# Performance work log

Hardware: AMD Instinct MI355X
Metric: run time of the kernel (lower is better)

## Reference

```python
import jax, jax.numpy as jnp
import numpy as np

N_NODES = 100000
N_EDGES = 800000
IN_CH = 128
HID = 128
OUT_CH = 64


def setup_inputs() -> dict:
    key = jax.random.key(0)
    ks = jax.random.split(key, 8)
    x = jax.random.normal(ks[0], (N_NODES, IN_CH), dtype=jnp.float32)
    edge_index = jax.random.randint(ks[1], (2, N_EDGES), 0, N_NODES, dtype=jnp.int64)
    # GCNConv weights (Glorot) and zero biases
    def glorot(k, fan_in, fan_out):
        s = jnp.sqrt(6.0 / (fan_in + fan_out))
        return jax.random.uniform(k, (fan_in, fan_out), jnp.float32, -s, s)
    return {
        "x": x,
        "edge_index": edge_index,
        "W1": glorot(ks[2], IN_CH, HID), "b1": jnp.zeros((HID,), jnp.float32),
        "W2": glorot(ks[3], HID, HID),   "b2": jnp.zeros((HID,), jnp.float32),
        "W3": glorot(ks[4], HID, OUT_CH), "b3": jnp.zeros((OUT_CH,), jnp.float32),
    }


def _gcn_conv(h, W, b, src, dst, norm, self_norm, n_nodes):
    """PyG GCNConv: out = D^-1/2 (A+I) D^-1/2 (h W) + b.
    Self-loop contribution added densely (self_norm = dinv^2) to avoid
    appending N extra edges."""
    h = h @ W  # [N, F_out]
    msg = h[src] * norm[:, None]  # [E, F_out] gathered + normalized messages
    agg = jax.ops.segment_sum(msg, dst, num_segments=n_nodes)
    return agg + h * self_norm[:, None] + b


def reference(x, edge_index, W1, b1, W2, b2, W3, b3):
    n_nodes = x.shape[0]
    src = edge_index[0]
    dst = edge_index[1]
    # degrees with self-loops (edge weights = 1)
    deg = jax.ops.segment_sum(jnp.ones_like(src, dtype=x.dtype), dst,
                              num_segments=n_nodes) + 1.0
    dinv = jax.lax.rsqrt(deg)
    norm = dinv[src] * dinv[dst]   # per-edge symmetric normalization
    self_norm = dinv * dinv        # normalization of the i->i self loop

    h = jax.nn.relu(_gcn_conv(x, W1, b1, src, dst, norm, self_norm, n_nodes))
    # dropout is identity in eval mode (training=False)
    h = jax.nn.relu(_gcn_conv(h, W2, b2, src, dst, norm, self_norm, n_nodes))
    out = _gcn_conv(h, W3, b3, src, dst, norm, self_norm, n_nodes)
    return out
```

## Files before the change

### kernel.cpp

```cpp
#include <hip/hip_runtime.h>


#define IN_CH 128

typedef __attribute__((ext_vector_type(8))) short bf16x8;
typedef __attribute__((ext_vector_type(4))) float f32x4;

__device__ inline unsigned short f2bf_rne(float f) {
    unsigned u = __float_as_uint(f);
    unsigned r = (u + 0x7FFFu + ((u >> 16) & 1u)) >> 16;
    return (unsigned short)r;
}
__device__ inline float bf2f(unsigned short h) {
    return __uint_as_float(((unsigned)h) << 16);
}
__device__ inline float bf2f_lo(unsigned m) {
    return __uint_as_float(m << 16);
}
__device__ inline float bf2f_hi(unsigned m) {
    return __uint_as_float(m & 0xffff0000u);
}

__global__ __launch_bounds__(256) void cnt_k(const int* __restrict__ dst,
                                             int* __restrict__ cnt, int E) {
    int e = blockIdx.x * 256 + threadIdx.x;
    if (e < E) atomicAdd(&cnt[dst[e]], 1);
}

__global__ __launch_bounds__(256) void scan1_k(const int* __restrict__ cnt,
                                               int* __restrict__ bsum,
                                               float* __restrict__ dinv, int N) {
    __shared__ int s[256];
    int tid = threadIdx.x;
    int i = blockIdx.x * 256 + tid;
    int vr = (i < N) ? cnt[i] : 0;
    if (i < N) dinv[i] = rsqrtf((float)vr + 1.0f);
    s[tid] = (i < N) ? ((vr + 8) & ~7) : 0;
    __syncthreads();
    for (int off = 128; off > 0; off >>= 1) {
        if (tid < off) s[tid] += s[tid + off];
        __syncthreads();
    }
    if (tid == 0) bsum[blockIdx.x] = s[0];
}

__global__ __launch_bounds__(512) void scan2_k(int* __restrict__ bsum, int nb) {
    __shared__ int s[512];
    __shared__ int carry_s;
    int tid = threadIdx.x;
    if (tid == 0) carry_s = 0;
    __syncthreads();
    for (int base = 0; base < nb; base += 512) {
        int c = carry_s;
        int i = base + tid;
        int v = (i < nb) ? bsum[i] : 0;
        s[tid] = v;
        __syncthreads();
        for (int off = 1; off < 512; off <<= 1) {
            int t = (tid >= off) ? s[tid - off] : 0;
            __syncthreads();
            s[tid] += t;
            __syncthreads();
        }
        if (i < nb) bsum[i] = s[tid] - v + c;
        __syncthreads();
        if (tid == 0) carry_s = c + s[511];
        __syncthreads();
    }
}

__global__ __launch_bounds__(256) void scan3_k(const int* __restrict__ cnt,
                                               const int* __restrict__ bsum,
                                               int* __restrict__ rowstart,
                                               int* __restrict__ cur, int N) {
    __shared__ int s[256];
    int tid = threadIdx.x;
    int i = blockIdx.x * 256 + tid;
    int v = (i < N) ? ((cnt[i] + 8) & ~7) : 0;
    s[tid] = v;
    __syncthreads();
    for (int off = 1; off < 256; off <<= 1) {
        int t = (tid >= off) ? s[tid - off] : 0;
        __syncthreads();
        s[tid] += t;
        __syncthreads();
    }
    if (i < N) {
        int st = s[tid] - v + bsum[blockIdx.x];
        rowstart[i] = st;
        cur[i] = st;
        if (i == N - 1) rowstart[N] = st + v;
    }
}

__device__ inline void convw_one(const float* W, unsigned short* hi, int FOUT, int id) {
    int n = id >> 7, k = id & 127;
    hi[id] = f2bf_rne(W[k * FOUT + n]);
}

__global__ __launch_bounds__(256) void fill_conv_k(
    const int* __restrict__ src, const int* __restrict__ dst,
    const float* __restrict__ dinv, int* __restrict__ cur,
    int2* __restrict__ pairs, int E, int N, int fillBlocks, int selfBlocks,
    int rangeSz,
    const float* __restrict__ W1, const float* __restrict__ W2,
    const float* __restrict__ W3,
    unsigned short* __restrict__ W1h, unsigned short* __restrict__ W2h,
    unsigned short* __restrict__ W3h) {
    if ((int)blockIdx.x < fillBlocks) {
        const int range = blockIdx.x & 7;
        const int lo = range * rangeSz;
        const int hi = lo + rangeSz;
        const int e0 = (blockIdx.x >> 3) * 1024 + threadIdx.x * 4;
        if (e0 >= E) return;
        int s[4], d[4];
        if (e0 + 4 <= E) {
            int4 s4 = *(const int4*)(src + e0);
            int4 d4 = *(const int4*)(dst + e0);
            s[0] = s4.x; s[1] = s4.y; s[2] = s4.z; s[3] = s4.w;
            d[0] = d4.x; d[1] = d4.y; d[2] = d4.z; d[3] = d4.w;
        } else {
#pragma unroll
            for (int k = 0; k < 4; ++k) {
                s[k] = (e0 + k < E) ? src[e0 + k] : 0;
                d[k] = (e0 + k < E) ? dst[e0 + k] : -1;
            }
        }
#pragma unroll
        for (int k = 0; k < 4; ++k) {
            if (d[k] >= lo && d[k] < hi) {
                float nrm = dinv[s[k]] * dinv[d[k]];
                int pos = atomicAdd(&cur[d[k]], 1);
                pairs[pos] = make_int2(s[k] * 256, __float_as_int(nrm));
            }
        }
    } else if ((int)blockIdx.x < fillBlocks + selfBlocks) {
        int i = (blockIdx.x - fillBlocks) * 256 + threadIdx.x;
        if (i < N) {
            float di = dinv[i];
            int pos = atomicAdd(&cur[i], 1);
            pairs[pos] = make_int2(i * 256, __float_as_int(di * di));
        }
    } else {
        int id = (blockIdx.x - fillBlocks - selfBlocks) * 256 + threadIdx.x;
        if (id < 16384) convw_one(W1, W1h, 128, id);
        else if (id < 32768) convw_one(W2, W2h, 128, id - 16384);
        else if (id < 40960) convw_one(W3, W3h, 64, id - 32768);
    }
}

__device__ inline bf16x8 cvt8(const float* __restrict__ p) {
    float4 v0 = *(const float4*)p;
    float4 v1 = *(const float4*)(p + 4);
    bf16x8 h;
    h[0] = (short)f2bf_rne(v0.x); h[1] = (short)f2bf_rne(v0.y);
    h[2] = (short)f2bf_rne(v0.z); h[3] = (short)f2bf_rne(v0.w);
    h[4] = (short)f2bf_rne(v1.x); h[5] = (short)f2bf_rne(v1.y);
    h[6] = (short)f2bf_rne(v1.z); h[7] = (short)f2bf_rne(v1.w);
    return h;
}

template <int FOUT, bool AF32>
__global__ __launch_bounds__(256) void mfma_gemm(const float* __restrict__ Af,
                                                 const unsigned short* __restrict__ Ahi,
                                                 const unsigned short* __restrict__ Bhi,
                                                 unsigned short* __restrict__ Thi,
                                                 int N) {
    constexpr int NCT = FOUT / 16;
    constexpr int BSTRIDE = 136;
    constexpr int CSTRIDE = FOUT + 8;
    constexpr int BU = FOUT * BSTRIDE;
    constexpr int CU = 64 * CSTRIDE;
    constexpr int SMEMU = (BU > CU) ? BU : CU;
    __shared__ unsigned short smem[SMEMU];

    const int tid = threadIdx.x;
    const int wv = tid >> 6, lane = tid & 63;
    const int quad = lane >> 4, l16 = lane & 15;
    const int row0 = blockIdx.x * 64 + wv * 16;

#pragma unroll
    for (int it = 0; it < FOUT / 16; ++it) {
        int i = it * 256 + tid;
        int r = i >> 4, c = (i & 15) * 8;
        *(bf16x8*)(&smem[r * BSTRIDE + c]) = *(const bf16x8*)(Bhi + (size_t)r * 128 + c);
    }
    __syncthreads();

    f32x4 acc[NCT];
#pragma unroll
    for (int ct = 0; ct < NCT; ++ct)
        acc[ct] = (f32x4){0.f, 0.f, 0.f, 0.f};

    const int ra = AF32 ? min(row0 + l16, N - 1) : (row0 + l16);

#pragma unroll
    for (int ks = 0; ks < 4; ++ks) {
        const int ko = ks * 32 + quad * 8;
        bf16x8 ah;
        if (AF32) {
            ah = cvt8(Af + (size_t)ra * 128 + ko);
        } else {
            ah = *(const bf16x8*)(Ahi + (size_t)ra * 128 + ko);
        }
#pragma unroll
        for (int ct = 0; ct < NCT; ++ct) {
            bf16x8 bh = *(const bf16x8*)(&smem[(ct * 16 + l16) * BSTRIDE + ko]);
            acc[ct] = __builtin_amdgcn_mfma_f32_16x16x32_bf16(ah, bh, acc[ct], 0, 0, 0);
        }
    }

    __syncthreads();
    const int lrow = wv * 16 + quad * 4;
#pragma unroll
    for (int ct = 0; ct < NCT; ++ct) {
        const int col = ct * 16 + l16;
#pragma unroll
        for (int r = 0; r < 4; ++r)
            smem[(lrow + r) * CSTRIDE + col] = f2bf_rne(acc[ct][r]);
    }
    __syncthreads();
    constexpr int CH = FOUT / 8;
#pragma unroll
    for (int i = 0; i < 64 * CH / 256; ++i) {
        int ci = i * 256 + tid;
        int r = ci / CH, c = (ci % CH) * 8;
        int grow = blockIdx.x * 64 + r;
        if (grow < N)
            *(uint4*)(Thi + (size_t)grow * FOUT + c) = *(const uint4*)&smem[r * CSTRIDE + c];
    }
}

struct Pairs4 { int4 p0, p1, p2, p3; };

__device__ inline Pairs4 ldpairs(const int2* __restrict__ pairs, int j) {
    Pairs4 r;
    r.p0 = *(const int4*)(pairs + j);
    r.p1 = *(const int4*)(pairs + j + 2);
    r.p2 = *(const int4*)(pairs + j + 4);
    r.p3 = *(const int4*)(pairs + j + 6);
    return r;
}

__device__ inline void ldrows128(const char* __restrict__ tbase, int laneB,
                                 const Pairs4& P, unsigned m[8]) {
    m[0] = *(const unsigned*)(tbase + (unsigned)P.p0.x + laneB);
    m[1] = *(const unsigned*)(tbase + (unsigned)P.p0.z + laneB);
    m[2] = *(const unsigned*)(tbase + (unsigned)P.p1.x + laneB);
    m[3] = *(const unsigned*)(tbase + (unsigned)P.p1.z + laneB);
    m[4] = *(const unsigned*)(tbase + (unsigned)P.p2.x + laneB);
    m[5] = *(const unsigned*)(tbase + (unsigned)P.p2.z + laneB);
    m[6] = *(const unsigned*)(tbase + (unsigned)P.p3.x + laneB);
    m[7] = *(const unsigned*)(tbase + (unsigned)P.p3.z + laneB);
}

__device__ inline void fma8_128(const Pairs4& P, const unsigned m[8],
                                float& ax, float& ay) {
    float n0 = __int_as_float(P.p0.y), n1 = __int_as_float(P.p0.w);
    float n2 = __int_as_float(P.p1.y), n3 = __int_as_float(P.p1.w);
    float n4 = __int_as_float(P.p2.y), n5 = __int_as_float(P.p2.w);
    float n6 = __int_as_float(P.p3.y), n7 = __int_as_float(P.p3.w);
    ax += n0 * bf2f_lo(m[0]); ay += n0 * bf2f_hi(m[0]);
    ax += n1 * bf2f_lo(m[1]); ay += n1 * bf2f_hi(m[1]);
    ax += n2 * bf2f_lo(m[2]); ay += n2 * bf2f_hi(m[2]);
    ax += n3 * bf2f_lo(m[3]); ay += n3 * bf2f_hi(m[3]);
    ax += n4 * bf2f_lo(m[4]); ay += n4 * bf2f_hi(m[4]);
    ax += n5 * bf2f_lo(m[5]); ay += n5 * bf2f_hi(m[5]);
    ax += n6 * bf2f_lo(m[6]); ay += n6 * bf2f_hi(m[6]);
    ax += n7 * bf2f_lo(m[7]); ay += n7 * bf2f_hi(m[7]);
}

__device__ inline void ldrows64(const char* __restrict__ tbase, int laneB,
                                const Pairs4& P, float m[8]) {
    m[0] = bf2f(*(const unsigned short*)(tbase + ((unsigned)P.p0.x >> 1) + laneB));
    m[1] = bf2f(*(const unsigned short*)(tbase + ((unsigned)P.p0.z >> 1) + laneB));
    m[2] = bf2f(*(const unsigned short*)(tbase + ((unsigned)P.p1.x >> 1) + laneB));
    m[3] = bf2f(*(const unsigned short*)(tbase + ((unsigned)P.p1.z >> 1) + laneB));
    m[4] = bf2f(*(const unsigned short*)(tbase + ((unsigned)P.p2.x >> 1) + laneB));
    m[5] = bf2f(*(const unsigned short*)(tbase + ((unsigned)P.p2.z >> 1) + laneB));
    m[6] = bf2f(*(const unsigned short*)(tbase + ((unsigned)P.p3.x >> 1) + laneB));
    m[7] = bf2f(*(const unsigned short*)(tbase + ((unsigned)P.p3.z >> 1) + laneB));
}

__device__ inline void fma8_64(const Pairs4& P, const float m[8], float& acc) {
    acc += __int_as_float(P.p0.y) * m[0] + __int_as_float(P.p0.w) * m[1] +
           __int_as_float(P.p1.y) * m[2] + __int_as_float(P.p1.w) * m[3] +
           __int_as_float(P.p2.y) * m[4] + __int_as_float(P.p2.w) * m[5] +
           __int_as_float(P.p3.y) * m[6] + __int_as_float(P.p3.w) * m[7];
}

template <int FOUT, bool SPLIT>
__global__ __launch_bounds__(256) void gather_k(const int* __restrict__ rowstart,
                                                const int2* __restrict__ pairs,
                                                const unsigned short* __restrict__ Thi,
                                                const float* __restrict__ bias,
                                                float* __restrict__ out,
                                                unsigned short* __restrict__ outHi,
                                                int N) {
    const int wave = threadIdx.x >> 6;
    const int lane = threadIdx.x & 63;
    const int rowA = blockIdx.x * 8 + wave * 2;
    if (rowA >= N) return;
    const int rowB = rowA + 1;
    const bool hasB = rowB < N;

    int2 se = *(const int2*)(rowstart + rowA);
    const int startA = se.x, endA = se.y;
    const int startB = endA;
    const int endB = hasB ? rowstart[rowA + 2] : startB;
    const char* tbase = (const char*)Thi;

    int itA = (endA - startA) >> 3;
    int itB = (endB - startB) >> 3;
    const int c = min(itA, itB);

    if (FOUT == 128) {
        const int laneB = lane * 4;
        float2 bb = *(const float2*)(bias + lane * 2);
        float axA = bb.x, ayA = bb.y, axB = bb.x, ayB = bb.y;

        Pairs4 PA = ldpairs(pairs, startA);
        Pairs4 PB = {};
        if (hasB) PB = ldpairs(pairs, startB);
        int jA = startA, jB = startB;

        for (int t = 0; t < c; ++t) {
            unsigned mA[8], mB[8];
            ldrows128(tbase, laneB, PA, mA);
            ldrows128(tbase, laneB, PB, mB);
            jA += 8; jB += 8;
            Pairs4 QA = ldpairs(pairs, jA);
            Pairs4 QB = ldpairs(pairs, jB);
            fma8_128(PA, mA, axA, ayA);
            fma8_128(PB, mB, axB, ayB);
            PA = QA; PB = QB;
        }
        for (int t = c; t < itA; ++t) {
            unsigned mA[8];
            ldrows128(tbase, laneB, PA, mA);
            jA += 8;
            Pairs4 QA = ldpairs(pairs, jA);
            fma8_128(PA, mA, axA, ayA);
            PA = QA;
        }
        for (int t = c; t < itB; ++t) {
            unsigned mB[8];
            ldrows128(tbase, laneB, PB, mB);
            jB += 8;
            Pairs4 QB = ldpairs(pairs, jB);
            fma8_128(PB, mB, axB, ayB);
            PB = QB;
        }

        if (SPLIT) {
            ushort2 hA;
            hA.x = f2bf_rne(fmaxf(axA, 0.f));
            hA.y = f2bf_rne(fmaxf(ayA, 0.f));
            *(ushort2*)(outHi + (size_t)rowA * 128 + lane * 2) = hA;
            if (hasB) {
                ushort2 hB;
                hB.x = f2bf_rne(fmaxf(axB, 0.f));
                hB.y = f2bf_rne(fmaxf(ayB, 0.f));
                *(ushort2*)(outHi + (size_t)rowB * 128 + lane * 2) = hB;
            }
        } else {
            float2 oA; oA.x = axA; oA.y = ayA;
            *(float2*)(out + (size_t)rowA * 128 + lane * 2) = oA;
            if (hasB) {
                float2 oB; oB.x = axB; oB.y = ayB;
                *(float2*)(out + (size_t)rowB * 128 + lane * 2) = oB;
            }
        }
    } else {
        const int laneB = lane * 2;
        const float bb = bias[lane];
        float accA = bb, accB = bb;

        Pairs4 PA = ldpairs(pairs, startA);
        Pairs4 PB = {};
        if (hasB) PB = ldpairs(pairs, startB);
        int jA = startA, jB = startB;

        for (int t = 0; t < c; ++t) {
            float mA[8], mB[8];
            ldrows64(tbase, laneB, PA, mA);
            ldrows64(tbase, laneB, PB, mB);
            jA += 8; jB += 8;
            Pairs4 QA = ldpairs(pairs, jA);
            Pairs4 QB = ldpairs(pairs, jB);
            fma8_64(PA, mA, accA);
            fma8_64(PB, mB, accB);
            PA = QA; PB = QB;
        }
        for (int t = c; t < itA; ++t) {
            float mA[8];
            ldrows64(tbase, laneB, PA, mA);
            jA += 8;
            Pairs4 QA = ldpairs(pairs, jA);
            fma8_64(PA, mA, accA);
            PA = QA;
        }
        for (int t = c; t < itB; ++t) {
            float mB[8];
            ldrows64(tbase, laneB, PB, mB);
            jB += 8;
            Pairs4 QB = ldpairs(pairs, jB);
            fma8_64(PB, mB, accB);
            PB = QB;
        }

        out[(size_t)rowA * FOUT + lane] = accA;
        if (hasB) out[(size_t)rowB * FOUT + lane] = accB;
    }
}

extern "C" void kernel_launch(void* const* d_in, const int* in_sizes, int n_in,
                              void* d_out, int out_size, void* d_ws, size_t ws_size,
                              hipStream_t stream) {
    const float* x  = (const float*)d_in[0];
    const int* eidx = (const int*)d_in[1];
    const float* W1 = (const float*)d_in[2];
    const float* b1 = (const float*)d_in[3];
    const float* W2 = (const float*)d_in[4];
    const float* b2 = (const float*)d_in[5];
    const float* W3 = (const float*)d_in[6];
    const float* b3 = (const float*)d_in[7];
    float* out = (float*)d_out;

    const int N = in_sizes[0] / IN_CH;
    const int E = in_sizes[1] / 2;
    const int* src = eidx;
    const int* dst = eidx + E;
    const int Npad = ((N + 127) / 128) * 128;
    const int nb = (N + 255) / 256;
    const int Emax = E + 8 * N + 24;

    auto align = [](size_t v) { return (v + 255) / 256 * 256; };
    char* p = (char*)d_ws;
    int* cnt = (int*)p;            p += align((size_t)N * 4);
    int* rowstart = (int*)p;       p += align((size_t)(N + 1) * 4);
    int* cur = (int*)p;            p += align((size_t)N * 4);
    int* bsum = (int*)p;           p += align((size_t)nb * 4);
    float* dinv = (float*)p;       p += align((size_t)N * 4);
    int2* pairs = (int2*)p;        p += align((size_t)Emax * 8);
    unsigned short* Ahi = (unsigned short*)p;  p += align((size_t)Npad * 128 * 2);
    unsigned short* Thi = (unsigned short*)p;  p += align((size_t)Npad * 128 * 2);
    unsigned short* W1h = (unsigned short*)p;  p += align(128 * 128 * 2);
    unsigned short* W2h = (unsigned short*)p;  p += align(128 * 128 * 2);
    unsigned short* W3h = (unsigned short*)p;

    hipMemsetAsync(cnt, 0, (size_t)N * 4, stream);
    hipMemsetAsync(pairs, 0, (size_t)Emax * 8, stream);
    cnt_k<<<(E + 255) / 256, 256, 0, stream>>>(dst, cnt, E);
    scan1_k<<<nb, 256, 0, stream>>>(cnt, bsum, dinv, N);
    scan2_k<<<1, 512, 0, stream>>>(bsum, nb);
    scan3_k<<<nb, 256, 0, stream>>>(cnt, bsum, rowstart, cur, N);
    const int chunks = (E + 1023) / 1024;
    const int fillBlocks = chunks * 8;
    const int selfBlocks = (N + 255) / 256;
    const int rangeSz = (N + 7) / 8;
    fill_conv_k<<<fillBlocks + selfBlocks + 160, 256, 0, stream>>>(
        src, dst, dinv, cur, pairs, E, N, fillBlocks, selfBlocks, rangeSz,
        W1, W2, W3, W1h, W2h, W3h);

    const int gemm_blocks = (N + 63) / 64;
    const int gather_blocks = (N + 7) / 8;

    mfma_gemm<128, true><<<gemm_blocks, 256, 0, stream>>>(x, nullptr, W1h, Thi, N);
    gather_k<128, true><<<gather_blocks, 256, 0, stream>>>(rowstart, pairs, Thi,
                                                           b1, nullptr, Ahi, N);
    mfma_gemm<128, false><<<gemm_blocks, 256, 0, stream>>>(nullptr, Ahi, W2h, Thi, N);
    gather_k<128, true><<<gather_blocks, 256, 0, stream>>>(rowstart, pairs, Thi,
                                                           b2, nullptr, Ahi, N);
    mfma_gemm<64, false><<<gemm_blocks, 256, 0, stream>>>(nullptr, Ahi, W3h, Thi, N);
    gather_k<64, false><<<gather_blocks, 256, 0, stream>>>(rowstart, pairs, Thi,
                                                           b3, out, nullptr, N);
}
```

Baseline: 350.6 us.

## Fuse first GEMM with CSR fill and make gather grid-stride

```diff
diff --git a/kernel.cpp b/kernel.cpp
--- a/kernel.cpp
+++ b/kernel.cpp
@@ -21,10 +21,26 @@
     return __uint_as_float(m & 0xffff0000u);
 }
 
-__global__ __launch_bounds__(256) void cnt_k(const int* __restrict__ dst,
-                                             int* __restrict__ cnt, int E) {
-    int e = blockIdx.x * 256 + threadIdx.x;
-    if (e < E) atomicAdd(&cnt[dst[e]], 1);
+__device__ inline void convw_one(const float* W, unsigned short* hi, int FOUT, int id) {
+    int n = id >> 7, k = id & 127;
+    hi[id] = f2bf_rne(W[k * FOUT + n]);
+}
+
+__global__ __launch_bounds__(256) void cntconv_k(
+    const int* __restrict__ dst, int* __restrict__ cnt, int E, int cntBlocks,
+    const float* __restrict__ W1, const float* __restrict__ W2,
+    const float* __restrict__ W3,
+    unsigned short* __restrict__ W1h, unsigned short* __restrict__ W2h,
+    unsigned short* __restrict__ W3h) {
+    if ((int)blockIdx.x < cntBlocks) {
+        int e = blockIdx.x * 256 + threadIdx.x;
+        if (e < E) atomicAdd(&cnt[dst[e]], 1);
+    } else {
+        int id = (blockIdx.x - cntBlocks) * 256 + threadIdx.x;
+        if (id < 16384) convw_one(W1, W1h, 128, id);
+        else if (id < 32768) convw_one(W2, W2h, 128, id - 16384);
+        else if (id < 40960) convw_one(W3, W3h, 64, id - 32768);
+    }
 }
 
 __global__ __launch_bounds__(256) void scan1_k(const int* __restrict__ cnt,
@@ -93,62 +109,6 @@
     }
 }
 
-__device__ inline void convw_one(const float* W, unsigned short* hi, int FOUT, int id) {
-    int n = id >> 7, k = id & 127;
-    hi[id] = f2bf_rne(W[k * FOUT + n]);
-}
-
-__global__ __launch_bounds__(256) void fill_conv_k(
-    const int* __restrict__ src, const int* __restrict__ dst,
-    const float* __restrict__ dinv, int* __restrict__ cur,
-    int2* __restrict__ pairs, int E, int N, int fillBlocks, int selfBlocks,
-    int rangeSz,
-    const float* __restrict__ W1, const float* __restrict__ W2,
-    const float* __restrict__ W3,
-    unsigned short* __restrict__ W1h, unsigned short* __restrict__ W2h,
-    unsigned short* __restrict__ W3h) {
-    if ((int)blockIdx.x < fillBlocks) {
-        const int range = blockIdx.x & 7;
-        const int lo = range * rangeSz;
-        const int hi = lo + rangeSz;
-        const int e0 = (blockIdx.x >> 3) * 1024 + threadIdx.x * 4;
-        if (e0 >= E) return;
-        int s[4], d[4];
-        if (e0 + 4 <= E) {
-            int4 s4 = *(const int4*)(src + e0);
-            int4 d4 = *(const int4*)(dst + e0);
-            s[0] = s4.x; s[1] = s4.y; s[2] = s4.z; s[3] = s4.w;
-            d[0] = d4.x; d[1] = d4.y; d[2] = d4.z; d[3] = d4.w;
-        } else {
-#pragma unroll
-            for (int k = 0; k < 4; ++k) {
-                s[k] = (e0 + k < E) ? src[e0 + k] : 0;
-                d[k] = (e0 + k < E) ? dst[e0 + k] : -1;
-            }
-        }
-#pragma unroll
-        for (int k = 0; k < 4; ++k) {
-            if (d[k] >= lo && d[k] < hi) {
-                float nrm = dinv[s[k]] * dinv[d[k]];
-                int pos = atomicAdd(&cur[d[k]], 1);
-                pairs[pos] = make_int2(s[k] * 256, __float_as_int(nrm));
-            }
-        }
-    } else if ((int)blockIdx.x < fillBlocks + selfBlocks) {
-        int i = (blockIdx.x - fillBlocks) * 256 + threadIdx.x;
-        if (i < N) {
-            float di = dinv[i];
-            int pos = atomicAdd(&cur[i], 1);
-            pairs[pos] = make_int2(i * 256, __float_as_int(di * di));
-        }
-    } else {
-        int id = (blockIdx.x - fillBlocks - selfBlocks) * 256 + threadIdx.x;
-        if (id < 16384) convw_one(W1, W1h, 128, id);
-        else if (id < 32768) convw_one(W2, W2h, 128, id - 16384);
-        else if (id < 40960) convw_one(W3, W3h, 64, id - 32768);
-    }
-}
-
 __device__ inline bf16x8 cvt8(const float* __restrict__ p) {
     float4 v0 = *(const float4*)p;
     float4 v1 = *(const float4*)(p + 4);
@@ -161,23 +121,19 @@
 }
 
 template <int FOUT, bool AF32>
-__global__ __launch_bounds__(256) void mfma_gemm(const float* __restrict__ Af,
-                                                 const unsigned short* __restrict__ Ahi,
-                                                 const unsigned short* __restrict__ Bhi,
-                                                 unsigned short* __restrict__ Thi,
-                                                 int N) {
+__device__ inline void gemm_body(int bid, const float* __restrict__ Af,
+                                 const unsigned short* __restrict__ Ahi,
+                                 const unsigned short* __restrict__ Bhi,
+                                 unsigned short* __restrict__ Thi, int N,
+                                 unsigned short* smem) {
     constexpr int NCT = FOUT / 16;
     constexpr int BSTRIDE = 136;
     constexpr int CSTRIDE = FOUT + 8;
-    constexpr int BU = FOUT * BSTRIDE;
-    constexpr int CU = 64 * CSTRIDE;
-    constexpr int SMEMU = (BU > CU) ? BU : CU;
-    __shared__ unsigned short smem[SMEMU];
 
     const int tid = threadIdx.x;
     const int wv = tid >> 6, lane = tid & 63;
     const int quad = lane >> 4, l16 = lane & 15;
-    const int row0 = blockIdx.x * 64 + wv * 16;
+    const int row0 = bid * 64 + wv * 16;
 
 #pragma unroll
     for (int it = 0; it < FOUT / 16; ++it) {
@@ -225,9 +181,72 @@
     for (int i = 0; i < 64 * CH / 256; ++i) {
         int ci = i * 256 + tid;
         int r = ci / CH, c = (ci % CH) * 8;
-        int grow = blockIdx.x * 64 + r;
+        int grow = bid * 64 + r;
         if (grow < N)
             *(uint4*)(Thi + (size_t)grow * FOUT + c) = *(const uint4*)&smem[r * CSTRIDE + c];
+    }
+}
+
+template <int FOUT, bool AF32>
+__global__ __launch_bounds__(256) void mfma_gemm(const float* __restrict__ Af,
+                                                 const unsigned short* __restrict__ Ahi,
+                                                 const unsigned short* __restrict__ Bhi,
+                                                 unsigned short* __restrict__ Thi,
+                                                 int N) {
+    constexpr int BU = FOUT * 136;
+    constexpr int CU2 = 64 * (FOUT + 8);
+    constexpr int SMEMU = (BU > CU2) ? BU : CU2;
+    __shared__ unsigned short smem[SMEMU];
+    gemm_body<FOUT, AF32>(blockIdx.x, Af, Ahi, Bhi, Thi, N, smem);
+}
+
+__global__ __launch_bounds__(256) void fillgemm_k(
+    const int* __restrict__ src, const int* __restrict__ dst,
+    const float* __restrict__ dinv, int* __restrict__ cur,
+    int2* __restrict__ pairs, int E, int N, int gemmBlocks, int fillBlocks,
+    int rangeSz,
+    const float* __restrict__ x, const unsigned short* __restrict__ W1h,
+    unsigned short* __restrict__ Thi) {
+    __shared__ unsigned short smem[128 * 136];
+    if ((int)blockIdx.x < gemmBlocks) {
+        gemm_body<128, true>(blockIdx.x, x, nullptr, W1h, Thi, N, smem);
+        return;
+    }
+    const int fb = blockIdx.x - gemmBlocks;
+    if (fb < fillBlocks) {
+        const int range = fb & 7;
+        const int lo = range * rangeSz;
+        const int hi = lo + rangeSz;
+        const int e0 = (fb >> 3) * 1024 + threadIdx.x * 4;
+        if (e0 >= E) return;
+        int s[4], d[4];
+        if (e0 + 4 <= E) {
+            int4 s4 = *(const int4*)(src + e0);
+            int4 d4 = *(const int4*)(dst + e0);
+            s[0] = s4.x; s[1] = s4.y; s[2] = s4.z; s[3] = s4.w;
+            d[0] = d4.x; d[1] = d4.y; d[2] = d4.z; d[3] = d4.w;
+        } else {
+#pragma unroll
+            for (int k = 0; k < 4; ++k) {
+                s[k] = (e0 + k < E) ? src[e0 + k] : 0;
+                d[k] = (e0 + k < E) ? dst[e0 + k] : -1;
+            }
+        }
+#pragma unroll
+        for (int k = 0; k < 4; ++k) {
+            if (d[k] >= lo && d[k] < hi) {
+                float nrm = dinv[s[k]] * dinv[d[k]];
+                int pos = atomicAdd(&cur[d[k]], 1);
+                pairs[pos] = make_int2(s[k] * 256, __float_as_int(nrm));
+            }
+        }
+    } else {
+        int i = (fb - fillBlocks) * 256 + threadIdx.x;
+        if (i < N) {
+            float di = dinv[i];
+            int pos = atomicAdd(&cur[i], 1);
+            pairs[pos] = make_int2(i * 256, __float_as_int(di * di));
+        }
     }
 }
 
@@ -299,118 +318,73 @@
                                                 int N) {
     const int wave = threadIdx.x >> 6;
     const int lane = threadIdx.x & 63;
-    const int rowA = blockIdx.x * 8 + wave * 2;
-    if (rowA >= N) return;
-    const int rowB = rowA + 1;
-    const bool hasB = rowB < N;
-
-    int2 se = *(const int2*)(rowstart + rowA);
-    const int startA = se.x, endA = se.y;
-    const int startB = endA;
-    const int endB = hasB ? rowstart[rowA + 2] : startB;
+    const int GW = gridDim.x * 4;
+    int row = blockIdx.x * 4 + wave;
+    if (row >= N) return;
     const char* tbase = (const char*)Thi;
 
-    int itA = (endA - startA) >> 3;
-    int itB = (endB - startB) >> 3;
-    const int c = min(itA, itB);
+    int sC = rowstart[row];
+    int eC = rowstart[row + 1];
+    Pairs4 P = ldpairs(pairs, sC);
 
     if (FOUT == 128) {
         const int laneB = lane * 4;
-        float2 bb = *(const float2*)(bias + lane * 2);
-        float axA = bb.x, ayA = bb.y, axB = bb.x, ayB = bb.y;
-
-        Pairs4 PA = ldpairs(pairs, startA);
-        Pairs4 PB = {};
-        if (hasB) PB = ldpairs(pairs, startB);
-        int jA = startA, jB = startB;
-
-        for (int t = 0; t < c; ++t) {
-            unsigned mA[8], mB[8];
-            ldrows128(tbase, laneB, PA, mA);
-            ldrows128(tbase, laneB, PB, mB);
-            jA += 8; jB += 8;
-            Pairs4 QA = ldpairs(pairs, jA);
-            Pairs4 QB = ldpairs(pairs, jB);
-            fma8_128(PA, mA, axA, ayA);
-            fma8_128(PB, mB, axB, ayB);
-            PA = QA; PB = QB;
-        }
-        for (int t = c; t < itA; ++t) {
-            unsigned mA[8];
-            ldrows128(tbase, laneB, PA, mA);
-            jA += 8;
-            Pairs4 QA = ldpairs(pairs, jA);
-            fma8_128(PA, mA, axA, ayA);
-            PA = QA;
-        }
-        for (int t = c; t < itB; ++t) {
-            unsigned mB[8];
-            ldrows128(tbase, laneB, PB, mB);
-            jB += 8;
-            Pairs4 QB = ldpairs(pairs, jB);
-            fma8_128(PB, mB, axB, ayB);
-            PB = QB;
-        }
-
-        if (SPLIT) {
-            ushort2 hA;
-            hA.x = f2bf_rne(fmaxf(axA, 0.f));
-            hA.y = f2bf_rne(fmaxf(ayA, 0.f));
-            *(ushort2*)(outHi + (size_t)rowA * 128 + lane * 2) = hA;
-            if (hasB) {
-                ushort2 hB;
-                hB.x = f2bf_rne(fmaxf(axB, 0.f));
-                hB.y = f2bf_rne(fmaxf(ayB, 0.f));
-                *(ushort2*)(outHi + (size_t)rowB * 128 + lane * 2) = hB;
+        const float2 bb = *(const float2*)(bias + lane * 2);
+        for (;;) {
+            const int nrow = row + GW;
+            const bool hasN = nrow < N;
+            int sN = sC, eN = eC;
+            if (hasN) { sN = rowstart[nrow]; eN = rowstart[nrow + 1]; }
+            float ax = bb.x, ay = bb.y;
+            int j = sC;
+            for (;;) {
+                unsigned m[8];
+                ldrows128(tbase, laneB, P, m);
+                j += 8;
+                const bool more = j < eC;
+                const int pj = more ? j : sN;
+                Pairs4 Q = ldpairs(pairs, pj);
+                fma8_128(P, m, ax, ay);
+                P = Q;
+                if (!more) break;
             }
-        } else {
-            float2 oA; oA.x = axA; oA.y = ayA;
-            *(float2*)(out + (size_t)rowA * 128 + lane * 2) = oA;
-            if (hasB) {
-                float2 oB; oB.x = axB; oB.y = ayB;
-                *(float2*)(out + (size_t)rowB * 128 + lane * 2) = oB;
+            if (SPLIT) {
+                ushort2 h;
+                h.x = f2bf_rne(fmaxf(ax, 0.f));
+                h.y = f2bf_rne(fmaxf(ay, 0.f));
+                *(ushort2*)(outHi + (size_t)row * 128 + lane * 2) = h;
+            } else {
+                float2 o; o.x = ax; o.y = ay;
+                *(float2*)(out + (size_t)row * 128 + lane * 2) = o;
             }
+            if (!hasN) break;
+            row = nrow; sC = sN; eC = eN;
         }
     } else {
         const int laneB = lane * 2;
         const float bb = bias[lane];
-        float accA = bb, accB = bb;
-
-        Pairs4 PA = ldpairs(pairs, startA);
-        Pairs4 PB = {};
-        if (hasB) PB = ldpairs(pairs, startB);
-        int jA = startA, jB = startB;
-
-        for (int t = 0; t < c; ++t) {
-            float mA[8], mB[8];
-            ldrows64(tbase, laneB, PA, mA);
-            ldrows64(tbase, laneB, PB, mB);
-            jA += 8; jB += 8;
-            Pairs4 QA = ldpairs(pairs, jA);
-            Pairs4 QB = ldpairs(pairs, jB);
-            fma8_64(PA, mA, accA);
-            fma8_64(PB, mB, accB);
-            PA = QA; PB = QB;
-        }
-        for (int t = c; t < itA; ++t) {
-            float mA[8];
-            ldrows64(tbase, laneB, PA, mA);
-            jA += 8;
-            Pairs4 QA = ldpairs(pairs, jA);
-            fma8_64(PA, mA, accA);
-            PA = QA;
-        }
-        for (int t = c; t < itB; ++t) {
-            float mB[8];
-            ldrows64(tbase, laneB, PB, mB);
-            jB += 8;
-            Pairs4 QB = ldpairs(pairs, jB);
-            fma8_64(PB, mB, accB);
-            PB = QB;
-        }
-
-        out[(size_t)rowA * FOUT + lane] = accA;
-        if (hasB) out[(size_t)rowB * FOUT + lane] = accB;
+        for (;;) {
+            const int nrow = row + GW;
+            const bool hasN = nrow < N;
+            int sN = sC, eN = eC;
+            if (hasN) { sN = rowstart[nrow]; eN = rowstart[nrow + 1]; }
+            float acc = bb;
+            int j = sC;
+            for (;;) {
+                float m[8];
+                ldrows64(tbase, laneB, P, m);
+                j += 8;
+                const bool more = j < eC;
+                const int pj = more ? j : sN;
+                Pairs4 Q = ldpairs(pairs, pj);
+                fma8_64(P, m, acc);
+                P = Q;
+                if (!more) break;
+            }
+            out[(size_t)row * FOUT + lane] = acc;
+            if (!hasN) break;
+            row = nrow; sC = sN; eC = eN;
+        }
     }
 }
 
@@ -451,22 +425,24 @@
 
     hipMemsetAsync(cnt, 0, (size_t)N * 4, stream);
     hipMemsetAsync(pairs, 0, (size_t)Emax * 8, stream);
-    cnt_k<<<(E + 255) / 256, 256, 0, stream>>>(dst, cnt, E);
+    const int cntBlocks = (E + 255) / 256;
+    cntconv_k<<<cntBlocks + 160, 256, 0, stream>>>(dst, cnt, E, cntBlocks,
+                                                   W1, W2, W3, W1h, W2h, W3h);
     scan1_k<<<nb, 256, 0, stream>>>(cnt, bsum, dinv, N);
     scan2_k<<<1, 512, 0, stream>>>(bsum, nb);
     scan3_k<<<nb, 256, 0, stream>>>(cnt, bsum, rowstart, cur, N);
+
+    const int gemm_blocks = (N + 63) / 64;
     const int chunks = (E + 1023) / 1024;
     const int fillBlocks = chunks * 8;
     const int selfBlocks = (N + 255) / 256;
     const int rangeSz = (N + 7) / 8;
-    fill_conv_k<<<fillBlocks + selfBlocks + 160, 256, 0, stream>>>(
-        src, dst, dinv, cur, pairs, E, N, fillBlocks, selfBlocks, rangeSz,
-        W1, W2, W3, W1h, W2h, W3h);
-
-    const int gemm_blocks = (N + 63) / 64;
-    const int gather_blocks = (N + 7) / 8;
-
-    mfma_gemm<128, true><<<gemm_blocks, 256, 0, stream>>>(x, nullptr, W1h, Thi, N);
+    fillgemm_k<<<gemm_blocks + fillBlocks + selfBlocks, 256, 0, stream>>>(
+        src, dst, dinv, cur, pairs, E, N, gemm_blocks, fillBlocks, rangeSz,
+        x, W1h, Thi);
+
+    const int gather_blocks = min(2048, (N + 3) / 4);
+
     gather_k<128, true><<<gather_blocks, 256, 0, stream>>>(rowstart, pairs, Thi,
                                                            b1, nullptr, Ahi, N);
     mfma_gemm<128, false><<<gemm_blocks, 256, 0, stream>>>(nullptr, Ahi, W2h, Thi, N);
```

Result: faster. 329.9 us (-5.9%).
